# Kernel optimization log

Hardware: AMD Instinct MI355X
Metric: run time of the kernel (lower is better)

Reference implementation:

```python
import jax, jax.numpy as jnp
import numpy as np

EMB = 1024
HEADS = 16

def setup_inputs() -> dict:
    key = jax.random.key(0)
    ks = jax.random.split(key, 9)
    s = 1.0 / np.sqrt(EMB)
    x = jax.random.normal(ks[0], (2, 2048, EMB), dtype=jnp.float32)
    Wq = jax.random.normal(ks[1], (EMB, EMB), dtype=jnp.float32) * s
    bq = jax.random.normal(ks[2], (EMB,), dtype=jnp.float32) * s
    Wk = jax.random.normal(ks[3], (EMB, EMB), dtype=jnp.float32) * s
    bk = jax.random.normal(ks[4], (EMB,), dtype=jnp.float32) * s
    Wv = jax.random.normal(ks[5], (EMB, EMB), dtype=jnp.float32) * s
    bv = jax.random.normal(ks[6], (EMB,), dtype=jnp.float32) * s
    Wo = jax.random.normal(ks[7], (EMB, EMB), dtype=jnp.float32) * s
    bo = jax.random.normal(ks[8], (EMB,), dtype=jnp.float32) * s
    return {"x": x, "Wq": Wq, "bq": bq, "Wk": Wk, "bk": bk, "Wv": Wv, "bv": bv, "Wo": Wo, "bo": bo}

def reference(x, Wq, bq, Wk, bk, Wv, bv, Wo, bo):
    B, N, E = x.shape
    H = HEADS
    D = E // H
    # q/k/v projections, split heads: b n (h d) -> b h n d
    def proj(W, b):
        y = jnp.einsum('bne,ef->bnf', x, W.T) + b
        return y.reshape(B, N, H, D).transpose(0, 2, 1, 3)
    q = proj(Wq, bq)
    k = proj(Wk, bk)
    v = proj(Wv, bv)
    energy = jnp.einsum('bhqd,bhkd->bhqk', q, k)
    scaling = jnp.asarray(E, x.dtype) ** 0.5  # note: sqrt(emb_size), as in source
    att = jax.nn.softmax(energy / scaling, axis=-1)
    out = jnp.einsum('bhqk,bhkd->bhqd', att, v)
    out = out.transpose(0, 2, 1, 3).reshape(B, N, E)  # b h n d -> b n (h d)
    return jnp.einsum('bne,ef->bnf', out, Wo.T) + bo
```

## Files before the change

### kernel.cpp

```cpp
#include <hip/hip_runtime.h>
#include <hip/hip_bf16.h>
#include <stdint.h>

typedef __bf16 bf16;
typedef __bf16 bf16x8 __attribute__((ext_vector_type(8)));
typedef __bf16 bf16x4 __attribute__((ext_vector_type(4)));
typedef __bf16 bf16x2 __attribute__((ext_vector_type(2)));
typedef float  f32x4  __attribute__((ext_vector_type(4)));
typedef float  f32x16 __attribute__((ext_vector_type(16)));
typedef unsigned int uint;

#define MFMA(a,b,c)   __builtin_amdgcn_mfma_f32_16x16x32_bf16((a),(b),(c),0,0,0)
#define MFMA32(a,b,c) __builtin_amdgcn_mfma_f32_32x32x16_bf16((a),(b),(c),0,0,0)
#define EXP2(x)       __builtin_amdgcn_exp2f(x)

__device__ __forceinline__ void gload_lds16(const void* g, void* lds) {
  __builtin_amdgcn_global_load_lds(
      (const __attribute__((address_space(1))) uint32_t*)g,
      (__attribute__((address_space(3))) uint32_t*)lds, 16, 0, 0);
}

__device__ __forceinline__ uint pk_bf16(float lo, float hi) {
  bf16x2 v; v[0] = (bf16)lo; v[1] = (bf16)hi;
  return __builtin_bit_cast(uint, v);
}

__global__ __launch_bounds__(256) void k_cvt(
    const float* __restrict__ x,
    const float* __restrict__ wq, const float* __restrict__ wk,
    const float* __restrict__ wv, const float* __restrict__ wo,
    bf16* __restrict__ xb, bf16* __restrict__ wqb, bf16* __restrict__ wkb,
    bf16* __restrict__ wvb, bf16* __restrict__ wob)
{
  int r = blockIdx.y;
  const float* s; bf16* d; int n;
  switch (r) {
    case 0: s = x;  d = xb;  n = 4194304; break;
    case 1: s = wq; d = wqb; n = 1048576; break;
    case 2: s = wk; d = wkb; n = 1048576; break;
    case 3: s = wv; d = wvb; n = 1048576; break;
    default: s = wo; d = wob; n = 1048576; break;
  }
  int i = (blockIdx.x * 256 + threadIdx.x) * 8;
  if (i >= n) return;
  const float4* sp = (const float4*)(s + i);
  float4 a = sp[0], b = sp[1];
  bf16x8 o;
  o[0]=(bf16)a.x; o[1]=(bf16)a.y; o[2]=(bf16)a.z; o[3]=(bf16)a.w;
  o[4]=(bf16)b.x; o[5]=(bf16)b.y; o[6]=(bf16)b.z; o[7]=(bf16)b.w;
  *(bf16x8*)(d + i) = o;
}

__global__ __launch_bounds__(256, 2) void k_gemm_qkv(
    const bf16* __restrict__ A,
    const bf16* __restrict__ Wq, const bf16* __restrict__ Wk, const bf16* __restrict__ Wv,
    const float* __restrict__ bq, const float* __restrict__ bk, const float* __restrict__ bv,
    bf16* __restrict__ Qw, bf16* __restrict__ Kw, bf16* __restrict__ Vtw)
{
  __shared__ __align__(16) char As[2][8192];
  __shared__ __align__(16) char Bs[2][8192];
  int tid = threadIdx.x;
  int wv4 = tid >> 6, l = tid & 63, lo = l & 15, hi = l >> 4;
  int f = blockIdx.y * 32 + blockIdx.x;
  int xcd = f & 7, i8 = f >> 3;
  int mt = xcd * 4 + (i8 & 3);
  int ft = i8 >> 2;
  int wsel = ft >> 3;
  const bf16* W = (wsel == 0) ? Wq : (wsel == 1) ? Wk : Wv;
  const float* bias = (wsel == 0) ? bq : (wsel == 1) ? bk : bv;
  int f0 = (ft & 7) * 128;
  const bf16* Ab = A + (size_t)mt * 128 * 1024;
  const bf16* Wb = W + (size_t)f0 * 1024;
  const bf16* Pa = (wsel < 2) ? Wb : Ab;
  const bf16* Pb = (wsel < 2) ? Ab : Wb;
  int wm = wv4 >> 1, wf = wv4 & 1;
  f32x4 acc[4][4];
  #pragma unroll
  for (int i = 0; i < 4; i++)
    #pragma unroll
    for (int j = 0; j < 4; j++) acc[i][j] = (f32x4){0.f, 0.f, 0.f, 0.f};

  #define STAGEG(t, bi) {                                              \
    int k0 = (t) * 32;                                                 \
    _Pragma("unroll")                                                  \
    for (int p = 0; p < 2; p++) {                                      \
      int sp = p * 256 + tid;                                          \
      int row = sp >> 2, s = sp & 3;                                   \
      int gc = k0 + 8 * (s ^ ((row >> 1) & 3));                        \
      gload_lds16(Pa + (size_t)row * 1024 + gc, As[bi] + sp * 16);     \
      gload_lds16(Pb + (size_t)row * 1024 + gc, Bs[bi] + sp * 16);     \
    } }

  STAGEG(0, 0);
  for (int t = 0; t < 32; ++t) {
    __syncthreads();
    if (t < 31) STAGEG(t + 1, (t + 1) & 1);
    const char* Ac = As[t & 1];
    const char* Bc = Bs[t & 1];
    bf16x8 af[4], bfr[4];
    #pragma unroll
    for (int ms = 0; ms < 4; ms++) {
      int row = wm * 64 + ms * 16 + lo;
      af[ms] = *(const bf16x8*)(Ac + row * 64 + 16 * (hi ^ ((row >> 1) & 3)));
    }
    #pragma unroll
    for (int fs = 0; fs < 4; fs++) {
      int row = wf * 64 + fs * 16 + lo;
      bfr[fs] = *(const bf16x8*)(Bc + row * 64 + 16 * (hi ^ ((row >> 1) & 3)));
    }
    __builtin_amdgcn_s_setprio(1);
    #pragma unroll
    for (int ms = 0; ms < 4; ms++)
      #pragma unroll
      for (int fs = 0; fs < 4; fs++)
        acc[ms][fs] = MFMA(af[ms], bfr[fs], acc[ms][fs]);
    __builtin_amdgcn_s_setprio(0);
  }
  #undef STAGEG

  if (wsel < 2) {
    bf16* Outp = (wsel == 0) ? Qw : Kw;
    float qs = (wsel == 0) ? 0.0450842199527801f : 1.0f;
    #pragma unroll
    for (int ms = 0; ms < 4; ms++) {
      int fl = f0 + wm * 64 + ms * 16 + hi * 4;
      int h = fl >> 6, dd = fl & 63;
      float4 b4 = *(const float4*)(bias + fl);
      #pragma unroll
      for (int fs = 0; fs < 4; fs++) {
        int m = mt * 128 + wf * 64 + fs * 16 + lo;
        int b = m >> 11, nn = m & 2047;
        bf16x4 w;
        #pragma unroll
        for (int r = 0; r < 4; r++)
          w[r] = (bf16)((acc[ms][fs][r] + ((const float*)&b4)[r]) * qs);
        *(bf16x4*)(Outp + (((size_t)(b * 16 + h) * 2048 + nn) * 64) + dd) = w;
      }
    }
  } else {
    #pragma unroll
    for (int fs = 0; fs < 4; fs++) {
      int fl = f0 + wf * 64 + fs * 16 + lo;
      int h = fl >> 6, dd = fl & 63;
      float bb = bias[fl];
      #pragma unroll
      for (int ms = 0; ms < 4; ms++) {
        int m = mt * 128 + wm * 64 + ms * 16 + hi * 4;
        int b = m >> 11, nn = m & 2047;
        bf16x4 w;
        #pragma unroll
        for (int r = 0; r < 4; r++) w[r] = (bf16)(acc[ms][fs][r] + bb);
        *(bf16x4*)(Vtw + (((size_t)(b * 16 + h) * 64 + dd) * 2048) + nn) = w;
      }
    }
  }
}

__global__ __launch_bounds__(256, 2) void k_attn(
    const bf16* __restrict__ Q, const bf16* __restrict__ K,
    const bf16* __restrict__ Vt, bf16* __restrict__ O)
{
  __shared__ __align__(16) char Ks[4][8192];
  __shared__ __align__(16) char Vs[4][8192];
  int tid = threadIdx.x;
  int wid = tid >> 6, l = tid & 63;
  int lq = l & 31, hi1 = l >> 5;
  int qhalf = wid >> 1, kpar = wid & 1;
  int f = blockIdx.y * 16 + blockIdx.x;
  int xcd = f & 7, i8 = f >> 3;
  int bh = xcd * 4 + (i8 & 3);
  int qt = i8 >> 2;
  int q0 = qt * 128 + qhalf * 64;
  const bf16* Kb = K + (size_t)bh * 2048 * 64;
  const bf16* Vb = Vt + (size_t)bh * 64 * 2048;

  bf16x8 qf0[4], qf1[4];
  const bf16* Qb = Q + ((size_t)bh * 2048 + q0) * 64 + hi1 * 8;
  #pragma unroll
  for (int c = 0; c < 4; c++) {
    qf0[c] = *(const bf16x8*)(Qb + (size_t)lq * 64 + 16 * c);
    qf1[c] = *(const bf16x8*)(Qb + (size_t)(lq + 32) * 64 + 16 * c);
  }

  f32x16 o00, o01, o10, o11, zz;
  #pragma unroll
  for (int r = 0; r < 16; r++) { zz[r] = 0.f; o00[r] = 0.f; o01[r] = 0.f; o10[r] = 0.f; o11[r] = 0.f; }
  float ls0 = 0.f, ls1 = 0.f;

  int srow = tid >> 3, slot = tid & 7;
  int swz = 16 * (slot ^ (srow & 7));
  int swk = lq & 7;
  uint4 xk0, xk1, xv0, xv1;
  uint4 yk0, yk1, yv0, yv1;
  #define STAGEX(t) {                                                          \
    xk0 = *(const uint4*)(Kb + (size_t)((t)*64 + srow) * 64 + slot * 8);       \
    xk1 = *(const uint4*)(Kb + (size_t)((t)*64 + srow + 32) * 64 + slot * 8);  \
    xv0 = *(const uint4*)(Vb + (size_t)srow * 2048 + (t)*64 + slot * 8);       \
    xv1 = *(const uint4*)(Vb + (size_t)(srow + 32) * 2048 + (t)*64 + slot * 8); }
  #define STAGEY(t) {                                                          \
    yk0 = *(const uint4*)(Kb + (size_t)((t)*64 + srow) * 64 + slot * 8);       \
    yk1 = *(const uint4*)(Kb + (size_t)((t)*64 + srow + 32) * 64 + slot * 8);  \
    yv0 = *(const uint4*)(Vb + (size_t)srow * 2048 + (t)*64 + slot * 8);       \
    yv1 = *(const uint4*)(Vb + (size_t)(srow + 32) * 2048 + (t)*64 + slot * 8); }
  #define WRX(bi) {                                     \
    *(uint4*)(Ks[bi] + srow * 128 + swz)        = xk0;  \
    *(uint4*)(Ks[bi] + (srow + 32) * 128 + swz) = xk1;  \
    *(uint4*)(Vs[bi] + srow * 128 + swz)        = xv0;  \
    *(uint4*)(Vs[bi] + (srow + 32) * 128 + swz) = xv1; }
  #define WRY(bi) {                                     \
    *(uint4*)(Ks[bi] + srow * 128 + swz)        = yk0;  \
    *(uint4*)(Ks[bi] + (srow + 32) * 128 + swz) = yk1;  \
    *(uint4*)(Vs[bi] + srow * 128 + swz)        = yv0;  \
    *(uint4*)(Vs[bi] + (srow + 32) * 128 + swz) = yv1; }
  #define EXPSUM(S, T0, T1, T2, T3)                     \
    _Pragma("unroll")                                   \
    for (int r = 0; r < 16; r += 4) {                   \
      S[r]   = EXP2(S[r]);   T0 += S[r];                \
      S[r+1] = EXP2(S[r+1]); T1 += S[r+1];              \
      S[r+2] = EXP2(S[r+2]); T2 += S[r+2];              \
      S[r+3] = EXP2(S[r+3]); T3 += S[r+3];              \
    }
  #define PACK(dst, plo, phi)                                                \
    _Pragma("unroll")                                                        \
    for (int m = 0; m < 2; m++) {                                            \
      uint a0 = pk_bf16(plo[8*m+0], plo[8*m+1]);                             \
      uint b0 = pk_bf16(plo[8*m+4], plo[8*m+5]);                             \
      asm volatile("v_permlane32_swap_b32 %0, %1" : "+v"(a0), "+v"(b0));     \
      uint a1 = pk_bf16(plo[8*m+2], plo[8*m+3]);                             \
      uint b1 = pk_bf16(plo[8*m+6], plo[8*m+7]);                             \
      asm volatile("v_permlane32_swap_b32 %0, %1" : "+v"(a1), "+v"(b1));     \
      dst[m] = (uint4){a0, a1, b0, b1};                                      \
      uint c0 = pk_bf16(phi[8*m+0], phi[8*m+1]);                             \
      uint d0 = pk_bf16(phi[8*m+4], phi[8*m+5]);                             \
      asm volatile("v_permlane32_swap_b32 %0, %1" : "+v"(c0), "+v"(d0));     \
      uint c1 = pk_bf16(phi[8*m+2], phi[8*m+3]);                             \
      uint d1 = pk_bf16(phi[8*m+6], phi[8*m+7]);                             \
      asm volatile("v_permlane32_swap_b32 %0, %1" : "+v"(c1), "+v"(d1));     \
      dst[2+m] = (uint4){c0, c1, d0, d1};                                    \
    }

  STAGEX(0); STAGEY(1);
  WRX(0); WRY(2);
  STAGEX(2); STAGEY(3);

  for (int e = 0; e < 16; ++e) {
    __syncthreads();
    if (e < 15) {
      WRX((e + 1) & 1);
      WRY(2 + ((e + 1) & 1));
    }
    int bi = kpar ? (2 + (e & 1)) : (e & 1);
    const char* Kc = (const char*)Ks + (size_t)bi * 8192;
    const char* Vc = (const char*)Vs + (size_t)bi * 8192;

    bf16x8 kf0[4], kf1[4];
    #pragma unroll
    for (int c = 0; c < 4; c++) {
      kf0[c] = *(const bf16x8*)(Kc + lq * 128 + 16 * ((2*c + hi1) ^ swk));
      kf1[c] = *(const bf16x8*)(Kc + (32 + lq) * 128 + 16 * ((2*c + hi1) ^ swk));
    }
    __builtin_amdgcn_s_setprio(1);
    f32x16 s00 = MFMA32(kf0[0], qf0[0], zz);
    f32x16 s01 = MFMA32(kf1[0], qf0[0], zz);
    f32x16 s10 = MFMA32(kf0[0], qf1[0], zz);
    f32x16 s11 = MFMA32(kf1[0], qf1[0], zz);
    #pragma unroll
    for (int c = 1; c < 4; c++) {
      s00 = MFMA32(kf0[c], qf0[c], s00);
      s01 = MFMA32(kf1[c], qf0[c], s01);
      s10 = MFMA32(kf0[c], qf1[c], s10);
      s11 = MFMA32(kf1[c], qf1[c], s11);
    }
    __builtin_amdgcn_s_setprio(0);

    float t0 = 0.f, t1 = 0.f, t2 = 0.f, t3 = 0.f;
    float u0 = 0.f, u1 = 0.f, u2 = 0.f, u3 = 0.f;
    EXPSUM(s00, t0, t1, t2, t3);
    EXPSUM(s01, t0, t1, t2, t3);
    EXPSUM(s10, u0, u1, u2, u3);
    EXPSUM(s11, u0, u1, u2, u3);
    ls0 += (t0 + t1) + (t2 + t3);
    ls1 += (u0 + u1) + (u2 + u3);

    uint4 pf0[4], pf1[4];
    PACK(pf0, s00, s01);
    PACK(pf1, s10, s11);

    __builtin_amdgcn_s_setprio(1);
    #pragma unroll
    for (int c = 0; c < 4; c++) {
      bf16x8 vf0 = *(const bf16x8*)(Vc + lq * 128 + 16 * ((2*c + hi1) ^ swk));
      bf16x8 vf1 = *(const bf16x8*)(Vc + (32 + lq) * 128 + 16 * ((2*c + hi1) ^ swk));
      bf16x8 p0b = __builtin_bit_cast(bf16x8, pf0[c]);
      bf16x8 p1b = __builtin_bit_cast(bf16x8, pf1[c]);
      o00 = MFMA32(vf0, p0b, o00);
      o01 = MFMA32(vf1, p0b, o01);
      o10 = MFMA32(vf0, p1b, o10);
      o11 = MFMA32(vf1, p1b, o11);
    }
    __builtin_amdgcn_s_setprio(0);

    if (e < 14) { STAGEX(2 * e + 4); STAGEY(2 * e + 5); }
  }
  #undef STAGEX
  #undef STAGEY
  #undef WRX
  #undef WRY

  __syncthreads();
  float* sc = (float*)(qhalf ? (char*)Vs : (char*)Ks) + 68 * l;
  if (kpar == 1) {
    #pragma unroll
    for (int g = 0; g < 4; g++) {
      *(f32x4*)(sc + 4*g)      = (f32x4){o00[4*g], o00[4*g+1], o00[4*g+2], o00[4*g+3]};
      *(f32x4*)(sc + 16 + 4*g) = (f32x4){o01[4*g], o01[4*g+1], o01[4*g+2], o01[4*g+3]};
      *(f32x4*)(sc + 32 + 4*g) = (f32x4){o10[4*g], o10[4*g+1], o10[4*g+2], o10[4*g+3]};
      *(f32x4*)(sc + 48 + 4*g) = (f32x4){o11[4*g], o11[4*g+1], o11[4*g+2], o11[4*g+3]};
    }
    sc[64] = ls0; sc[65] = ls1;
  }
  __syncthreads();
  if (kpar == 0) {
    #pragma unroll
    for (int g = 0; g < 4; g++) {
      f32x4 a0 = *(const f32x4*)(sc + 4*g);
      f32x4 a1 = *(const f32x4*)(sc + 16 + 4*g);
      f32x4 a2 = *(const f32x4*)(sc + 32 + 4*g);
      f32x4 a3 = *(const f32x4*)(sc + 48 + 4*g);
      #pragma unroll
      for (int j = 0; j < 4; j++) {
        o00[4*g+j] += a0[j];
        o01[4*g+j] += a1[j];
        o10[4*g+j] += a2[j];
        o11[4*g+j] += a3[j];
      }
    }
    ls0 += sc[64]; ls1 += sc[65];
    float lA = ls0 + __shfl_xor(ls0, 32);
    float lB = ls1 + __shfl_xor(ls1, 32);
    float inv0 = 1.0f / lA, inv1 = 1.0f / lB;
    int b = bh >> 4, h = bh & 15;
    bf16* Ob0 = O + ((size_t)(b * 2048 + q0 + lq)) * 1024 + h * 64 + hi1 * 4;
    bf16* Ob1 = O + ((size_t)(b * 2048 + q0 + 32 + lq)) * 1024 + h * 64 + hi1 * 4;
    #pragma unroll
    for (int g = 0; g < 4; g++) {
      bf16x4 w0, w1, w2, w3;
      #pragma unroll
      for (int j = 0; j < 4; j++) {
        w0[j] = (bf16)(o00[4*g+j] * inv0);
        w1[j] = (bf16)(o01[4*g+j] * inv0);
        w2[j] = (bf16)(o10[4*g+j] * inv1);
        w3[j] = (bf16)(o11[4*g+j] * inv1);
      }
      *(bf16x4*)(Ob0 + g * 8)      = w0;
      *(bf16x4*)(Ob0 + 32 + g * 8) = w1;
      *(bf16x4*)(Ob1 + g * 8)      = w2;
      *(bf16x4*)(Ob1 + 32 + g * 8) = w3;
    }
  }
}

__global__ __launch_bounds__(512, 1) void k_gemm_out(
    const bf16* __restrict__ A,
    const bf16* __restrict__ W,
    const float* __restrict__ bias,
    float* __restrict__ Cout)
{
  __shared__ __align__(16) char As[2][16384];
  __shared__ __align__(16) char Bs[2][16384];
  int tid = threadIdx.x;
  int wid = tid >> 6, l = tid & 63, lo = l & 15, hi = l >> 4;
  int f = blockIdx.y * 32 + blockIdx.x;
  int xcd = f & 7, i8 = f >> 3;
  int mt = xcd * 4 + (i8 & 3);
  int f0 = (i8 >> 2) * 128;
  const bf16* Ab = A + (size_t)mt * 128 * 1024;
  const bf16* Wb = W + (size_t)f0 * 1024;
  int wm2 = wid >> 2, wf4 = wid & 3;
  f32x4 acc[2][4];
  #pragma unroll
  for (int i = 0; i < 2; i++)
    #pragma unroll
    for (int j = 0; j < 4; j++) acc[i][j] = (f32x4){0.f, 0.f, 0.f, 0.f};

  #define STAGEG(t, bi) {                                              \
    int k0 = (t) * 64;                                                 \
    _Pragma("unroll")                                                  \
    for (int p = 0; p < 2; p++) {                                      \
      int sp = p * 512 + tid;                                          \
      int row = sp >> 3, s = sp & 7;                                   \
      int gc = k0 + 8 * (s ^ (row & 7));                               \
      gload_lds16(Wb + (size_t)row * 1024 + gc, As[bi] + sp * 16);     \
      gload_lds16(Ab + (size_t)row * 1024 + gc, Bs[bi] + sp * 16);     \
    } }

  STAGEG(0, 0);
  for (int t = 0; t < 16; ++t) {
    __syncthreads();
    if (t < 15) STAGEG(t + 1, (t + 1) & 1);
    const char* Ac = As[t & 1];
    const char* Bc = Bs[t & 1];
    #pragma unroll
    for (int kk = 0; kk < 2; kk++) {
      bf16x8 wfr[2], afr[4];
      #pragma unroll
      for (int i = 0; i < 2; i++) {
        int row = wf4 * 32 + i * 16 + lo;
        wfr[i] = *(const bf16x8*)(Ac + row * 128 + 16 * ((kk * 4 + hi) ^ (row & 7)));
      }
      #pragma unroll
      for (int j = 0; j < 4; j++) {
        int row = wm2 * 64 + j * 16 + lo;
        afr[j] = *(const bf16x8*)(Bc + row * 128 + 16 * ((kk * 4 + hi) ^ (row & 7)));
      }
      __builtin_amdgcn_s_setprio(1);
      #pragma unroll
      for (int i = 0; i < 2; i++)
        #pragma unroll
        for (int j = 0; j < 4; j++)
          acc[i][j] = MFMA(wfr[i], afr[j], acc[i][j]);
      __builtin_amdgcn_s_setprio(0);
    }
  }
  #undef STAGEG

  #pragma unroll
  for (int i = 0; i < 2; i++) {
    int fl = f0 + wf4 * 32 + i * 16 + hi * 4;
    float4 b4 = *(const float4*)(bias + fl);
    #pragma unroll
    for (int j = 0; j < 4; j++) {
      int m = mt * 128 + wm2 * 64 + j * 16 + lo;
      float4 o;
      o.x = acc[i][j][0] + b4.x;
      o.y = acc[i][j][1] + b4.y;
      o.z = acc[i][j][2] + b4.z;
      o.w = acc[i][j][3] + b4.w;
      *(float4*)(Cout + (size_t)m * 1024 + fl) = o;
    }
  }
}

extern "C" void kernel_launch(void* const* d_in, const int* in_sizes, int n_in,
                              void* d_out, int out_size, void* d_ws, size_t ws_size,
                              hipStream_t stream) {
  const float* x  = (const float*)d_in[0];
  const float* Wq = (const float*)d_in[1];
  const float* bq = (const float*)d_in[2];
  const float* Wk = (const float*)d_in[3];
  const float* bk = (const float*)d_in[4];
  const float* Wv = (const float*)d_in[5];
  const float* bv = (const float*)d_in[6];
  const float* Wo = (const float*)d_in[7];
  const float* bo = (const float*)d_in[8];
  float* out = (float*)d_out;
  char* ws = (char*)d_ws;

  bf16* xb  = (bf16*)(ws);
  bf16* wqb = (bf16*)(ws + 8388608);
  bf16* wkb = (bf16*)(ws + 10485760);
  bf16* wvb = (bf16*)(ws + 12582912);
  bf16* wob = (bf16*)(ws + 14680064);
  bf16* Qw  = (bf16*)(ws + 16777216);
  bf16* Kw  = (bf16*)(ws + 25165824);
  bf16* Vtw = (bf16*)(ws + 33554432);
  bf16* Ow  = (bf16*)(ws + 41943040);

  k_cvt<<<dim3(2048, 5), 256, 0, stream>>>(x, Wq, Wk, Wv, Wo, xb, wqb, wkb, wvb, wob);
  k_gemm_qkv<<<dim3(32, 24), 256, 0, stream>>>(xb, wqb, wkb, wvb, bq, bk, bv, Qw, Kw, Vtw);
  k_attn<<<dim3(16, 32), 256, 0, stream>>>(Qw, Kw, Vtw, Ow);
  k_gemm_out<<<dim3(32, 8), 512, 0, stream>>>(Ow, wob, bo, out);
}
```

Baseline: 104.4 us.

## Triple-buffer QKV GEMM loads with vmcnt waits and compact conversion grid

The QKV projection GEMM moves from a double-buffered to a triple-buffered LDS pipeline, prefetching two k-tiles ahead. It synchronises with explicit vmcnt waits plus a raw barrier instead of __syncthreads, which is meant to hide global load latency behind the MFMA work. The conversion kernel's grid shrinks from 2048x5 to 4096 blocks, so the blocks that used to exit early on the smaller weight matrices are no longer launched. The risks are the larger LDS footprint (48KB per block) under a 3-block occupancy hint, and correctness that depends on the hand-counted vmcnt.

```diff
diff --git a/kernel.cpp b/kernel.cpp
--- a/kernel.cpp
+++ b/kernel.cpp
@@ -32,17 +32,20 @@
     bf16* __restrict__ xb, bf16* __restrict__ wqb, bf16* __restrict__ wkb,
     bf16* __restrict__ wvb, bf16* __restrict__ wob)
 {
-  int r = blockIdx.y;
-  const float* s; bf16* d; int n;
-  switch (r) {
-    case 0: s = x;  d = xb;  n = 4194304; break;
-    case 1: s = wq; d = wqb; n = 1048576; break;
-    case 2: s = wk; d = wkb; n = 1048576; break;
-    case 3: s = wv; d = wvb; n = 1048576; break;
-    default: s = wo; d = wob; n = 1048576; break;
-  }
-  int i = (blockIdx.x * 256 + threadIdx.x) * 8;
-  if (i >= n) return;
+  int bid = blockIdx.x;
+  const float* s; bf16* d; int base;
+  if (bid < 2048) { s = x; d = xb; base = bid; }
+  else {
+    int r = (bid - 2048) >> 9;
+    base = (bid - 2048) & 511;
+    switch (r) {
+      case 0: s = wq; d = wqb; break;
+      case 1: s = wk; d = wkb; break;
+      case 2: s = wv; d = wvb; break;
+      default: s = wo; d = wob; break;
+    }
+  }
+  int i = (base * 256 + threadIdx.x) * 8;
   const float4* sp = (const float4*)(s + i);
   float4 a = sp[0], b = sp[1];
   bf16x8 o;
@@ -51,14 +54,14 @@
   *(bf16x8*)(d + i) = o;
 }
 
-__global__ __launch_bounds__(256, 2) void k_gemm_qkv(
+__global__ __launch_bounds__(256, 3) void k_gemm_qkv(
     const bf16* __restrict__ A,
     const bf16* __restrict__ Wq, const bf16* __restrict__ Wk, const bf16* __restrict__ Wv,
     const float* __restrict__ bq, const float* __restrict__ bk, const float* __restrict__ bv,
     bf16* __restrict__ Qw, bf16* __restrict__ Kw, bf16* __restrict__ Vtw)
 {
-  __shared__ __align__(16) char As[2][8192];
-  __shared__ __align__(16) char Bs[2][8192];
+  __shared__ __align__(16) char As[3][8192];
+  __shared__ __align__(16) char Bs[3][8192];
   int tid = threadIdx.x;
   int wv4 = tid >> 6, l = tid & 63, lo = l & 15, hi = l >> 4;
   int f = blockIdx.y * 32 + blockIdx.x;
@@ -92,11 +95,16 @@
     } }
 
   STAGEG(0, 0);
+  STAGEG(1, 1);
   for (int t = 0; t < 32; ++t) {
-    __syncthreads();
-    if (t < 31) STAGEG(t + 1, (t + 1) & 1);
-    const char* Ac = As[t & 1];
-    const char* Bc = Bs[t & 1];
+    if (t < 31) asm volatile("s_waitcnt vmcnt(4)" ::: "memory");
+    else        asm volatile("s_waitcnt vmcnt(0)" ::: "memory");
+    __builtin_amdgcn_s_barrier();
+    __builtin_amdgcn_sched_barrier(0);
+    if (t < 30) { int bi2 = (t + 2) % 3; STAGEG(t + 2, bi2); }
+    int bi = t % 3;
+    const char* Ac = As[bi];
+    const char* Bc = Bs[bi];
     bf16x8 af[4], bfr[4];
     #pragma unroll
     for (int ms = 0; ms < 4; ms++) {
@@ -466,7 +474,7 @@
   bf16* Vtw = (bf16*)(ws + 33554432);
   bf16* Ow  = (bf16*)(ws + 41943040);
 
-  k_cvt<<<dim3(2048, 5), 256, 0, stream>>>(x, Wq, Wk, Wv, Wo, xb, wqb, wkb, wvb, wob);
+  k_cvt<<<dim3(4096), 256, 0, stream>>>(x, Wq, Wk, Wv, Wo, xb, wqb, wkb, wvb, wob);
   k_gemm_qkv<<<dim3(32, 24), 256, 0, stream>>>(xb, wqb, wkb, wvb, bq, bk, bv, Qw, Kw, Vtw);
   k_attn<<<dim3(16, 32), 256, 0, stream>>>(Qw, Kw, Vtw, Ow);
   k_gemm_out<<<dim3(32, 8), 512, 0, stream>>>(Ow, wob, bo, out);
```

New measurement: 105.3 us. About the same (+0.9%).
